# Optimization experiments

Hardware: AMD Instinct MI355X
Metric: run time of the kernel (lower is better)

Reference implementation:

```python
import jax, jax.numpy as jnp
import numpy as np

E = 1024          # embed_dim
BS = 8            # number of sequences (bs = pre_lf_indexs.shape[0])
L = 8192          # tokens per sequence
N = BS * L        # packed tokens
CACHE = 16384     # lf cache rows
EPS = 1e-6


def setup_inputs() -> dict:
    key = jax.random.key(0)
    ks = jax.random.split(key, 9)
    inputs = jax.random.normal(ks[0], (N, E), jnp.float32)
    conv1_weight = jax.random.normal(ks[1], (E, E), jnp.float32) * (1.0 / np.sqrt(E))
    conv2_weight = jax.random.normal(ks[2], (E // 2, 2 * E), jnp.float32) * (1.0 / np.sqrt(E // 2))
    conv1_bias = jax.random.normal(ks[3], (E // 2,), jnp.float32) * 0.02
    conv2_bias = jax.random.normal(ks[4], (E,), jnp.float32) * 0.02
    ln_weight = jnp.ones((E,), jnp.float32)
    lf1_caches = jax.random.normal(ks[5], (CACHE, E), jnp.float32)
    lf2_caches = jax.random.normal(ks[6], (CACHE, E // 2), jnp.float32)
    # packed layout: each sequence prefixed by one cache slot -> T = N + BS rows
    offs = jnp.arange(BS, dtype=jnp.int32) * (L + 1)
    input_lf_loc = offs                                             # cache slot per seq
    inputs_loc = (offs[:, None] + 1 + jnp.arange(L, dtype=jnp.int32)[None, :]).reshape(-1)
    outputs_loc = inputs_loc - 1                                     # 2-tap causal pairing
    out_lf_loc = offs + L                                            # last token of each seq
    pre_lf_indexs = jax.random.randint(ks[7], (BS,), 0, CACHE, jnp.int32)
    out_lf_indexs = jax.random.randint(ks[8], (BS,), 0, CACHE, jnp.int32)
    return {
        'inputs': inputs, 'conv1_weight': conv1_weight, 'conv2_weight': conv2_weight,
        'conv1_bias': conv1_bias, 'conv2_bias': conv2_bias, 'ln_weight': ln_weight,
        'lf1_caches': lf1_caches, 'lf2_caches': lf2_caches,
        'pre_lf_indexs': pre_lf_indexs, 'out_lf_indexs': out_lf_indexs,
        'input_lf_loc': input_lf_loc, 'out_lf_loc': out_lf_loc,
        'inputs_loc': inputs_loc, 'outputs_loc': outputs_loc,
    }


def _fused_cat_conv2d(x, cache, W, pre_idx, in_lf_loc, in_loc, out_loc):
    # scatter cache rows + token rows into the padded buffer [N+bs, D]
    T = x.shape[0] + pre_idx.shape[0]
    xt = jnp.zeros((T, x.shape[1]), x.dtype)
    xt = xt.at[in_lf_loc].set(cache[pre_idx])   # gather from lf cache
    xt = xt.at[in_loc].set(x)
    co = xt @ W                                  # [T, 2*Dout]
    h = co.shape[1] // 2
    # shifted 2-tap causal conv: pair row j (prev) with row j+1 (cur)
    ot = co[:-1, :h] + co[1:, h:]                # [T-1, Dout]
    return ot[out_loc]                           # gather back to token order


def reference(inputs, conv1_weight, conv2_weight, conv1_bias, conv2_bias, ln_weight,
              lf1_caches, lf2_caches, pre_lf_indexs, out_lf_indexs,
              input_lf_loc, out_lf_loc, inputs_loc, outputs_loc):
    # (the index_put_ cache writes in the original are side effects for future
    #  steps only; they do not affect this call's output, so they are omitted)
    output1 = _fused_cat_conv2d(inputs, lf1_caches, conv1_weight,
                                pre_lf_indexs, input_lf_loc, inputs_loc, outputs_loc)
    output1 = output1 + conv1_bias               # [N, E/2]
    output2 = _fused_cat_conv2d(output1, lf2_caches, conv2_weight,
                                pre_lf_indexs, input_lf_loc, inputs_loc, outputs_loc)
    output2 = output2 + conv2_bias               # [N, E]
    x = output2 + inputs                         # residual
    var = jnp.mean(x * x, axis=-1, keepdims=True)
    return x * jax.lax.rsqrt(var + EPS) * ln_weight
```

## Files before the change

### kernel.cpp

```cpp
#include <hip/hip_runtime.h>
#include <hip/hip_bf16.h>


#define EDIM 1024
#define HDIM 512
#define LSEQ 8192
#define BSEQ 8
#define SEQR 8193
#define MTOT (BSEQ * SEQR)
#define XROWS 66048

using v8s = __attribute__((ext_vector_type(8))) short;
using v4f = __attribute__((ext_vector_type(4))) float;

__device__ __forceinline__ unsigned short f2b(float f) {
  union { float f; unsigned u; } v; v.f = f;
  unsigned r = v.u + 0x7fffu + ((v.u >> 16) & 1u);
  return (unsigned short)(r >> 16);
}
__device__ __forceinline__ float b2f(unsigned short h) {
  union { unsigned u; float f; } v; v.u = ((unsigned)h) << 16; return v.f;
}
__device__ __forceinline__ void gl_lds16(const void* g, void* l) {
  __builtin_amdgcn_global_load_lds((const __attribute__((address_space(1))) void*)g,
                                   (__attribute__((address_space(3))) void*)l, 16, 0, 0);
}

__device__ __forceinline__ void trns64(const float* __restrict__ src, int src_ld, int src_c0,
                                       unsigned short* __restrict__ dst, int dst_ld, int dst_k0,
                                       int n0, int k0, float (*t)[65], int tx, int ty) {
#pragma unroll
  for (int yy = 0; yy < 64; yy += 4)
    t[yy + ty][tx] = src[(size_t)(k0 + yy + ty) * src_ld + src_c0 + n0 + tx];
  __syncthreads();
#pragma unroll
  for (int yy = 0; yy < 64; yy += 4)
    dst[(size_t)(n0 + yy + ty) * dst_ld + dst_k0 + k0 + tx] = f2b(t[tx][yy + ty]);
}

__global__ __launch_bounds__(256) void prep_all(const float* __restrict__ W1,
                                                const float* __restrict__ W2,
                                                const float* __restrict__ lf2,
                                                const int* __restrict__ preidx,
                                                unsigned short* __restrict__ W1c,
                                                unsigned short* __restrict__ W2c,
                                                unsigned short* __restrict__ c2b) {
  __shared__ float t[64][65];
  const int bk = blockIdx.x;
  const int tid = threadIdx.x;
  if (bk == 512) {
    for (int c = tid; c < HDIM; c += 256)
#pragma unroll
      for (int b = 0; b < BSEQ; ++b)
        c2b[b * HDIM + c] = f2b(lf2[(size_t)preidx[b] * HDIM + c]);
    return;
  }
  const int tx = tid & 63, ty = tid >> 6;
  const int which = bk >> 7, s = bk & 127;
  if (which == 0)       trns64(W1, 1024, 0,    W1c, 2048, 0,    (s & 7) * 64,  (s >> 3) * 64, t, tx, ty);
  else if (which == 1)  trns64(W1, 1024, 512,  W1c, 2048, 1024, (s & 7) * 64,  (s >> 3) * 64, t, tx, ty);
  else if (which == 2)  trns64(W2, 2048, 0,    W2c, 1024, 0,    (s & 15) * 64, (s >> 4) * 64, t, tx, ty);
  else                  trns64(W2, 2048, 1024, W2c, 1024, 512,  (s & 15) * 64, (s >> 4) * 64, t, tx, ty);
}

__global__ __launch_bounds__(256) void cvt_full(const float* __restrict__ inputs,
                                                const float* __restrict__ lf1,
                                                const int* __restrict__ preidx,
                                                unsigned short* __restrict__ Xbf) {
  const int r = blockIdx.x * 4 + (threadIdx.x >> 6);
  const int lane = threadIdx.x & 63;
  unsigned short* dst = Xbf + (size_t)r * EDIM;
  if (r >= MTOT) {
#pragma unroll
    for (int c = lane * 4; c < EDIM; c += 256)
      *(ushort4*)&dst[c] = (ushort4){0, 0, 0, 0};
    return;
  }
  const int b = r / SEQR, rr = r % SEQR;
  const float* src = (rr == 0) ? (lf1 + (size_t)preidx[b] * EDIM)
                               : (inputs + (size_t)(b * LSEQ + rr - 1) * EDIM);
#pragma unroll
  for (int c = lane * 4; c < EDIM; c += 256) {
    const float4 v = *(const float4*)(src + c);
    *(ushort4*)&dst[c] = (ushort4){f2b(v.x), f2b(v.y), f2b(v.z), f2b(v.w)};
  }
}

__global__ __launch_bounds__(512) void fixup_full(const unsigned short* __restrict__ Xbf,
                                                  const unsigned short* __restrict__ W1c,
                                                  const float* __restrict__ b1,
                                                  const unsigned short* __restrict__ c2b,
                                                  unsigned short* __restrict__ A2) {
  const int blk = blockIdx.x;
  const int tid = threadIdx.x;
  if (blk == 7) {
#pragma unroll
    for (int b = 0; b < BSEQ; ++b)
      A2[(size_t)(b * SEQR) * HDIM + tid] = c2b[b * HDIM + tid];
    return;
  }
  const int r = 65536 + blk;
  const unsigned short* a = Xbf + (size_t)r * EDIM;
  const unsigned short* wrow = W1c + (size_t)tid * 2048;
  float s = 0.f;
  for (int k = 0; k < 2048; k += 8) {
    const v8s av = *(const v8s*)&a[k];
    const v8s wv = *(const v8s*)&wrow[k];
#pragma unroll
    for (int j = 0; j < 8; ++j)
      s += b2f((unsigned short)av[j]) * b2f((unsigned short)wv[j]);
  }
  A2[(size_t)(r + 1) * HDIM + tid] = f2b(s + b1[tid]);
}

#define PHASE(p, boA_, off_, ra_)                                                      \
  {                                                                                    \
    v8s af[2][2];                                                                      \
    _Pragma("unroll") for (int m2 = 0; m2 < 2; ++m2)                                   \
    _Pragma("unroll") for (int kx = 0; kx < 2; ++kx)                                   \
      af[m2][kx] = *(const v8s*)&lds[(boA_) +                                          \
          ((2 * (p) + m2) * 32 + wm * 16 + lr + (off_)) * 64 +                         \
          (((kx * 4 + lk) ^ (ra_)) << 3)];                                             \
    __builtin_amdgcn_s_setprio(1);                                                     \
    _Pragma("unroll") for (int m2 = 0; m2 < 2; ++m2)                                   \
    _Pragma("unroll") for (int nc = 0; nc < 4; ++nc)                                   \
    _Pragma("unroll") for (int kx = 0; kx < 2; ++kx)                                   \
      acc[2 * (p) + m2][nc] = __builtin_amdgcn_mfma_f32_16x16x32_bf16(                 \
          af[m2][kx], bf[nc][kx], acc[2 * (p) + m2][nc], 0, 0, 0);                     \
    __builtin_amdgcn_s_setprio(0);                                                     \
  }

#define LOAD_BFR(boB_)                                                                 \
  _Pragma("unroll") for (int nc = 0; nc < 4; ++nc)                                     \
  _Pragma("unroll") for (int kx = 0; kx < 2; ++kx)                                     \
    bf[nc][kx] = *(const v8s*)&lds[(boB_) + (nc * 64 + wn * 16 + lr) * 64 +            \
                                   (((kx * 4 + lk) ^ ra7a) << 3)];

#define STEP4(boA_, off_, ra_)                                                         \
  PHASE(0, boA_, off_, ra_) PHASE(1, boA_, off_, ra_)                                  \
  PHASE(2, boA_, off_, ra_) PHASE(3, boA_, off_, ra_)

template <int K, int NT, bool SHIFTC, bool AMAP>
__global__ __launch_bounds__(512, 2) void gemm_pair(const unsigned short* __restrict__ A,
                                                    const unsigned short* __restrict__ B,
                                                    unsigned short* __restrict__ C,
                                                    const float* __restrict__ bias,
                                                    int q, int r) {
  constexpr int NH = K / 128;
  constexpr int LDA = K / 2;
  constexpr int N = NT * 256;
  constexpr int A0 = 0, A1 = 16512, B_A = 33024, B_B = 49408;
  __shared__ __align__(16) unsigned short lds[65792];

  const int h = blockIdx.x;
  const int xcd = h & 7, idx = h >> 3;
  const int tsw = (xcd < r ? xcd * (q + 1) : r * (q + 1) + (xcd - r) * q) + idx;
  const int mt = tsw / NT, nt = tsw % NT;
  const size_t m0 = (size_t)mt * 256, n0 = (size_t)nt * 256;
  const int tid = threadIdx.x;
  const int w = tid >> 6, lane = tid & 63;
  const int wm = w >> 2, wn = w & 3;
  const int lr = lane & 15, lk = lane >> 4;
  const int ra7a = lr & 7, ra7b = (lr + 1) & 7;
  const int srow = tid >> 3, slot = tid & 7;
  const int gslot = slot ^ (srow & 7);
  const int dAB = srow * 64 + slot * 8;
  const int aBase = (int)m0 + (AMAP ? ((int)m0 >> 13) : 0);

  auto stageApair = [&](int dstE, int i) {
#pragma unroll
    for (int j = 0; j < 4; ++j) {
      const int rr = j * 64 + (tid >> 3);
      gl_lds16(A + (size_t)(aBase + rr) * LDA + i * 64 + ((tid & 7) ^ (rr & 7)) * 8,
               &lds[dstE + rr * 64 + (tid & 7) * 8]);
    }
    if (tid < 8)
      gl_lds16(A + (size_t)(aBase + 256) * LDA + i * 64 + tid * 8,
               &lds[dstE + 256 * 64 + tid * 8]);
  };
  auto stageB = [&](int dstE, int hh, int t) {
    const unsigned short* s = B + (size_t)(n0 + hh * 128 + srow) * K + t * 64 + gslot * 8;
    unsigned short* d = &lds[dstE + hh * 8192 + dAB];
    gl_lds16(s, d);
    gl_lds16(s + (size_t)64 * K, d + 4096);
  };

  v4f acc[8][4];
#pragma unroll
  for (int i = 0; i < 8; ++i)
#pragma unroll
    for (int j = 0; j < 4; ++j) acc[i][j] = (v4f){0.f, 0.f, 0.f, 0.f};

  stageApair(A0, 0);
  stageB(B_A, 0, 0); stageB(B_A, 1, 0);
  asm volatile("s_waitcnt vmcnt(0)" ::: "memory");
  __builtin_amdgcn_s_barrier();

#pragma unroll 1
  for (int i = 0; i < NH - 1; ++i) {
    const int boA = (i & 1) ? A1 : A0;
    const int soA = (i & 1) ? A0 : A1;
    v8s bf[4][2];
    stageB(B_B, 0, i + NH); stageB(B_B, 1, i + NH);
    stageApair(soA, i + 1);
    LOAD_BFR(B_A)
    STEP4(boA, 0, ra7a)
    asm volatile("s_waitcnt vmcnt(4)" ::: "memory");
    __builtin_amdgcn_s_barrier();
    stageB(B_A, 0, i + 1); stageB(B_A, 1, i + 1);
    LOAD_BFR(B_B)
    STEP4(boA, 1, ra7b)
    asm volatile("s_waitcnt vmcnt(0)" ::: "memory");
    __builtin_amdgcn_s_barrier();
  }
  {
    const int boA = ((NH - 1) & 1) ? A1 : A0;
    v8s bf[4][2];
    stageB(B_B, 0, 2 * NH - 1); stageB(B_B, 1, 2 * NH - 1);
    LOAD_BFR(B_A)
    STEP4(boA, 0, ra7a)
    asm volatile("s_waitcnt vmcnt(0)" ::: "memory");
    __builtin_amdgcn_s_barrier();
    LOAD_BFR(B_B)
    STEP4(boA, 1, ra7b)
  }

#pragma unroll
  for (int mr = 0; mr < 8; ++mr)
#pragma unroll
    for (int nc = 0; nc < 4; ++nc) {
      const size_t col = n0 + nc * 64 + wn * 16 + lr;
      float bv = 0.f;
      if constexpr (SHIFTC) bv = bias[col];
#pragma unroll
      for (int g = 0; g < 4; ++g) {
        const size_t row = m0 + mr * 32 + wm * 16 + lk * 4 + g + (SHIFTC ? 1 : 0);
        C[row * N + col] = f2b(acc[mr][nc][g] + bv);
      }
    }
}

__global__ __launch_bounds__(256) void epilogue_full(
    const unsigned short* __restrict__ Zo, const unsigned short* __restrict__ Xbf,
    const float* __restrict__ b2, const float* __restrict__ lnw,
    float* __restrict__ out) {
  const int u = blockIdx.x;
  const size_t rx = (size_t)u + (u >> 13) + 1;
  const int tid = threadIdx.x;
  const int j0 = tid * 4;

  const ushort4 z = *(const ushort4*)&Zo[(size_t)u * EDIM + j0];
  const ushort4 xb = *(const ushort4*)&Xbf[rx * EDIM + j0];
  const float4 bb = *(const float4*)&b2[j0];
  const float4 lw = *(const float4*)&lnw[j0];

  const float x0 = b2f(z.x) + bb.x + b2f(xb.x);
  const float x1 = b2f(z.y) + bb.y + b2f(xb.y);
  const float x2 = b2f(z.z) + bb.z + b2f(xb.z);
  const float x3 = b2f(z.w) + bb.w + b2f(xb.w);

  float ss = x0 * x0 + x1 * x1 + x2 * x2 + x3 * x3;
#pragma unroll
  for (int o = 32; o > 0; o >>= 1) ss += __shfl_xor(ss, o, 64);
  __shared__ float sp[4];
  if ((tid & 63) == 0) sp[tid >> 6] = ss;
  __syncthreads();
  const float tot = sp[0] + sp[1] + sp[2] + sp[3];
  const float scale = rsqrtf(tot * (1.0f / EDIM) + 1e-6f);

  float4 o4;
  o4.x = x0 * scale * lw.x; o4.y = x1 * scale * lw.y;
  o4.z = x2 * scale * lw.z; o4.w = x3 * scale * lw.w;
  *(float4*)&out[(size_t)u * EDIM + j0] = o4;
}

extern "C" void kernel_launch(void* const* d_in, const int* in_sizes, int n_in,
                              void* d_out, int out_size, void* d_ws, size_t ws_size,
                              hipStream_t stream) {
  const float* inputs = (const float*)d_in[0];
  const float* W1 = (const float*)d_in[1];
  const float* W2 = (const float*)d_in[2];
  const float* b1 = (const float*)d_in[3];
  const float* b2 = (const float*)d_in[4];
  const float* lnw = (const float*)d_in[5];
  const float* lf1 = (const float*)d_in[6];
  const float* lf2 = (const float*)d_in[7];
  const int* preidx = (const int*)d_in[8];
  float* out = (float*)d_out;

  char* ws = (char*)d_ws;
  unsigned short* Xbf = (unsigned short*)(ws);
  unsigned short* A2  = (unsigned short*)(ws + 135266304ULL);
  unsigned short* Zo  = (unsigned short*)(ws + 202899456ULL);
  unsigned short* W1c = (unsigned short*)(ws + 337117184ULL);
  unsigned short* W2c = (unsigned short*)(ws + 339214336ULL);
  unsigned short* c2b = (unsigned short*)(ws + 341311488ULL);

  prep_all<<<513, 256, 0, stream>>>(W1, W2, lf2, preidx, W1c, W2c, c2b);
  cvt_full<<<XROWS / 4, 256, 0, stream>>>(inputs, lf1, preidx, Xbf);
  gemm_pair<2048, 2, true, false><<<512, 512, 0, stream>>>(Xbf, W1c, A2, b1, 64, 0);
  fixup_full<<<8, 512, 0, stream>>>(Xbf, W1c, b1, c2b, A2);
  gemm_pair<1024, 4, false, true><<<1024, 512, 0, stream>>>(A2, W2c, Zo, nullptr, 128, 0);
  epilogue_full<<<BSEQ * LSEQ, 256, 0, stream>>>(Zo, Xbf, b2, lnw, out);
}
```

Before: 471.5 us.

## Interleave global-to-LDS staging with MFMA phases using per-phase barriers

```diff
diff --git a/kernel.cpp b/kernel.cpp
--- a/kernel.cpp
+++ b/kernel.cpp
@@ -113,22 +113,12 @@
   A2[(size_t)(r + 1) * HDIM + tid] = f2b(s + b1[tid]);
 }
 
-#define PHASE(p, boA_, off_, ra_)                                                      \
-  {                                                                                    \
-    v8s af[2][2];                                                                      \
-    _Pragma("unroll") for (int m2 = 0; m2 < 2; ++m2)                                   \
-    _Pragma("unroll") for (int kx = 0; kx < 2; ++kx)                                   \
-      af[m2][kx] = *(const v8s*)&lds[(boA_) +                                          \
-          ((2 * (p) + m2) * 32 + wm * 16 + lr + (off_)) * 64 +                         \
-          (((kx * 4 + lk) ^ (ra_)) << 3)];                                             \
-    __builtin_amdgcn_s_setprio(1);                                                     \
-    _Pragma("unroll") for (int m2 = 0; m2 < 2; ++m2)                                   \
-    _Pragma("unroll") for (int nc = 0; nc < 4; ++nc)                                   \
-    _Pragma("unroll") for (int kx = 0; kx < 2; ++kx)                                   \
-      acc[2 * (p) + m2][nc] = __builtin_amdgcn_mfma_f32_16x16x32_bf16(                 \
-          af[m2][kx], bf[nc][kx], acc[2 * (p) + m2][nc], 0, 0, 0);                     \
-    __builtin_amdgcn_s_setprio(0);                                                     \
-  }
+#define LOAD_AFR(p, boA_, off_, ra_)                                                   \
+  _Pragma("unroll") for (int m2 = 0; m2 < 2; ++m2)                                     \
+  _Pragma("unroll") for (int kx = 0; kx < 2; ++kx)                                     \
+    af[m2][kx] = *(const v8s*)&lds[(boA_) +                                            \
+        ((2 * (p) + m2) * 32 + wm * 16 + lr + (off_)) * 64 +                           \
+        (((kx * 4 + lk) ^ (ra_)) << 3)];
 
 #define LOAD_BFR(boB_)                                                                 \
   _Pragma("unroll") for (int nc = 0; nc < 4; ++nc)                                     \
@@ -136,9 +126,22 @@
     bf[nc][kx] = *(const v8s*)&lds[(boB_) + (nc * 64 + wn * 16 + lr) * 64 +            \
                                    (((kx * 4 + lk) ^ ra7a) << 3)];
 
-#define STEP4(boA_, off_, ra_)                                                         \
-  PHASE(0, boA_, off_, ra_) PHASE(1, boA_, off_, ra_)                                  \
-  PHASE(2, boA_, off_, ra_) PHASE(3, boA_, off_, ra_)
+#define MFMA_CORE(p)                                                                   \
+  __builtin_amdgcn_s_barrier();                                                        \
+  asm volatile("s_waitcnt lgkmcnt(0)" ::: "memory");                                   \
+  __builtin_amdgcn_s_setprio(1);                                                       \
+  _Pragma("unroll") for (int m2 = 0; m2 < 2; ++m2)                                     \
+  _Pragma("unroll") for (int nc = 0; nc < 4; ++nc)                                     \
+  _Pragma("unroll") for (int kx = 0; kx < 2; ++kx)                                     \
+    acc[2 * (p) + m2][nc] = __builtin_amdgcn_mfma_f32_16x16x32_bf16(                   \
+        af[m2][kx], bf[nc][kx], acc[2 * (p) + m2][nc], 0, 0, 0);                       \
+  __builtin_amdgcn_s_setprio(0);
+
+#define MFMA_PH(p)    MFMA_CORE(p) __builtin_amdgcn_s_barrier();
+#define MFMA_PH_W5(p) MFMA_CORE(p)                                                     \
+  asm volatile("s_waitcnt vmcnt(5)" ::: "memory"); __builtin_amdgcn_s_barrier();
+#define MFMA_PH_W0(p) MFMA_CORE(p)                                                     \
+  asm volatile("s_waitcnt vmcnt(0)" ::: "memory"); __builtin_amdgcn_s_barrier();
 
 template <int K, int NT, bool SHIFTC, bool AMAP>
 __global__ __launch_bounds__(512, 2) void gemm_pair(const unsigned short* __restrict__ A,
@@ -167,16 +170,24 @@
   const int dAB = srow * 64 + slot * 8;
   const int aBase = (int)m0 + (AMAP ? ((int)m0 >> 13) : 0);
 
-  auto stageApair = [&](int dstE, int i) {
-#pragma unroll
-    for (int j = 0; j < 4; ++j) {
+  auto stageA01 = [&](int dstE, int i) {
+#pragma unroll
+    for (int j = 0; j < 2; ++j) {
       const int rr = j * 64 + (tid >> 3);
       gl_lds16(A + (size_t)(aBase + rr) * LDA + i * 64 + ((tid & 7) ^ (rr & 7)) * 8,
                &lds[dstE + rr * 64 + (tid & 7) * 8]);
     }
-    if (tid < 8)
-      gl_lds16(A + (size_t)(aBase + 256) * LDA + i * 64 + tid * 8,
-               &lds[dstE + 256 * 64 + tid * 8]);
+  };
+  auto stageA23t = [&](int dstE, int i) {
+#pragma unroll
+    for (int j = 2; j < 4; ++j) {
+      const int rr = j * 64 + (tid >> 3);
+      gl_lds16(A + (size_t)(aBase + rr) * LDA + i * 64 + ((tid & 7) ^ (rr & 7)) * 8,
+               &lds[dstE + rr * 64 + (tid & 7) * 8]);
+    }
+    if ((tid & 63) < 8)
+      gl_lds16(A + (size_t)(aBase + 256) * LDA + i * 64 + (tid & 7) * 8,
+               &lds[dstE + 256 * 64 + (tid & 7) * 8]);
   };
   auto stageB = [&](int dstE, int hh, int t) {
     const unsigned short* s = B + (size_t)(n0 + hh * 128 + srow) * K + t * 64 + gslot * 8;
@@ -191,7 +202,7 @@
 #pragma unroll
     for (int j = 0; j < 4; ++j) acc[i][j] = (v4f){0.f, 0.f, 0.f, 0.f};
 
-  stageApair(A0, 0);
+  stageA01(A0, 0); stageA23t(A0, 0);
   stageB(B_A, 0, 0); stageB(B_A, 1, 0);
   asm volatile("s_waitcnt vmcnt(0)" ::: "memory");
   __builtin_amdgcn_s_barrier();
@@ -200,29 +211,55 @@
   for (int i = 0; i < NH - 1; ++i) {
     const int boA = (i & 1) ? A1 : A0;
     const int soA = (i & 1) ? A0 : A1;
-    v8s bf[4][2];
-    stageB(B_B, 0, i + NH); stageB(B_B, 1, i + NH);
-    stageApair(soA, i + 1);
+    v8s bf[4][2], af[2][2];
     LOAD_BFR(B_A)
-    STEP4(boA, 0, ra7a)
-    asm volatile("s_waitcnt vmcnt(4)" ::: "memory");
-    __builtin_amdgcn_s_barrier();
-    stageB(B_A, 0, i + 1); stageB(B_A, 1, i + 1);
+    LOAD_AFR(0, boA, 0, ra7a)
+    stageB(B_B, 0, i + NH);
+    MFMA_PH(0)
+    LOAD_AFR(1, boA, 0, ra7a)
+    stageB(B_B, 1, i + NH);
+    MFMA_PH(1)
+    LOAD_AFR(2, boA, 0, ra7a)
+    stageA01(soA, i + 1);
+    MFMA_PH(2)
+    LOAD_AFR(3, boA, 0, ra7a)
+    stageA23t(soA, i + 1);
+    MFMA_PH_W5(3)
     LOAD_BFR(B_B)
-    STEP4(boA, 1, ra7b)
-    asm volatile("s_waitcnt vmcnt(0)" ::: "memory");
-    __builtin_amdgcn_s_barrier();
+    LOAD_AFR(0, boA, 1, ra7b)
+    stageB(B_A, 0, i + 1);
+    MFMA_PH(0)
+    LOAD_AFR(1, boA, 1, ra7b)
+    stageB(B_A, 1, i + 1);
+    MFMA_PH(1)
+    LOAD_AFR(2, boA, 1, ra7b)
+    MFMA_PH(2)
+    LOAD_AFR(3, boA, 1, ra7b)
+    MFMA_PH_W0(3)
   }
   {
     const int boA = ((NH - 1) & 1) ? A1 : A0;
-    v8s bf[4][2];
-    stageB(B_B, 0, 2 * NH - 1); stageB(B_B, 1, 2 * NH - 1);
+    v8s bf[4][2], af[2][2];
     LOAD_BFR(B_A)
-    STEP4(boA, 0, ra7a)
-    asm volatile("s_waitcnt vmcnt(0)" ::: "memory");
-    __builtin_amdgcn_s_barrier();
+    LOAD_AFR(0, boA, 0, ra7a)
+    stageB(B_B, 0, 2 * NH - 1);
+    MFMA_PH(0)
+    LOAD_AFR(1, boA, 0, ra7a)
+    stageB(B_B, 1, 2 * NH - 1);
+    MFMA_PH(1)
+    LOAD_AFR(2, boA, 0, ra7a)
+    MFMA_PH(2)
+    LOAD_AFR(3, boA, 0, ra7a)
+    MFMA_PH_W0(3)
     LOAD_BFR(B_B)
-    STEP4(boA, 1, ra7b)
+    LOAD_AFR(0, boA, 1, ra7b)
+    MFMA_PH(0)
+    LOAD_AFR(1, boA, 1, ra7b)
+    MFMA_PH(1)
+    LOAD_AFR(2, boA, 1, ra7b)
+    MFMA_PH(2)
+    LOAD_AFR(3, boA, 1, ra7b)
+    MFMA_PH(3)
   }
 
 #pragma unroll
```

Measured after the change: 475.3 us. Within noise of the previous version (+0.8%).

## Fuse fp32-to-bf16 input conversion and cache gather into first GEMM A-loading

Applied to the files above, without the earlier changes.

```diff
diff --git a/kernel.cpp b/kernel.cpp
--- a/kernel.cpp
+++ b/kernel.cpp
@@ -63,30 +63,7 @@
   else                  trns64(W2, 2048, 1024, W2c, 1024, 512,  (s & 15) * 64, (s >> 4) * 64, t, tx, ty);
 }
 
-__global__ __launch_bounds__(256) void cvt_full(const float* __restrict__ inputs,
-                                                const float* __restrict__ lf1,
-                                                const int* __restrict__ preidx,
-                                                unsigned short* __restrict__ Xbf) {
-  const int r = blockIdx.x * 4 + (threadIdx.x >> 6);
-  const int lane = threadIdx.x & 63;
-  unsigned short* dst = Xbf + (size_t)r * EDIM;
-  if (r >= MTOT) {
-#pragma unroll
-    for (int c = lane * 4; c < EDIM; c += 256)
-      *(ushort4*)&dst[c] = (ushort4){0, 0, 0, 0};
-    return;
-  }
-  const int b = r / SEQR, rr = r % SEQR;
-  const float* src = (rr == 0) ? (lf1 + (size_t)preidx[b] * EDIM)
-                               : (inputs + (size_t)(b * LSEQ + rr - 1) * EDIM);
-#pragma unroll
-  for (int c = lane * 4; c < EDIM; c += 256) {
-    const float4 v = *(const float4*)(src + c);
-    *(ushort4*)&dst[c] = (ushort4){f2b(v.x), f2b(v.y), f2b(v.z), f2b(v.w)};
-  }
-}
-
-__global__ __launch_bounds__(512) void fixup_full(const unsigned short* __restrict__ Xbf,
+__global__ __launch_bounds__(512) void fixup_full(const float* __restrict__ inputs,
                                                   const unsigned short* __restrict__ W1c,
                                                   const float* __restrict__ b1,
                                                   const unsigned short* __restrict__ c2b,
@@ -100,17 +77,174 @@
     return;
   }
   const int r = 65536 + blk;
-  const unsigned short* a = Xbf + (size_t)r * EDIM;
+  const float* x0 = inputs + (size_t)(r - 8) * EDIM;
+  const float* x1 = inputs + (size_t)(r - 7) * EDIM;
   const unsigned short* wrow = W1c + (size_t)tid * 2048;
   float s = 0.f;
-  for (int k = 0; k < 2048; k += 8) {
-    const v8s av = *(const v8s*)&a[k];
-    const v8s wv = *(const v8s*)&wrow[k];
-#pragma unroll
-    for (int j = 0; j < 8; ++j)
-      s += b2f((unsigned short)av[j]) * b2f((unsigned short)wv[j]);
+  for (int k = 0; k < 1024; k += 4) {
+    const float4 a = *(const float4*)(x0 + k);
+    const float4 c = *(const float4*)(x1 + k);
+    const ushort4 wa = *(const ushort4*)&wrow[k];
+    const ushort4 wc = *(const ushort4*)&wrow[1024 + k];
+    s += b2f(f2b(a.x)) * b2f(wa.x) + b2f(f2b(a.y)) * b2f(wa.y) +
+         b2f(f2b(a.z)) * b2f(wa.z) + b2f(f2b(a.w)) * b2f(wa.w);
+    s += b2f(f2b(c.x)) * b2f(wc.x) + b2f(f2b(c.y)) * b2f(wc.y) +
+         b2f(f2b(c.z)) * b2f(wc.z) + b2f(f2b(c.w)) * b2f(wc.w);
   }
   A2[(size_t)(r + 1) * HDIM + tid] = f2b(s + b1[tid]);
+}
+
+#define KX1(kx, boA_, off_, ra_, boB_)                                          \
+  {                                                                             \
+    v8s bfk[4], afk[2];                                                         \
+    _Pragma("unroll") for (int nc = 0; nc < 4; ++nc)                            \
+      bfk[nc] = *(const v8s*)&lds[(boB_) + (nc * 64 + wn * 16 + lr) * 64 +      \
+                                  ((((kx)*4 + lk) ^ ra7a) << 3)];               \
+    _Pragma("unroll") for (int p = 0; p < 4; ++p) {                             \
+      _Pragma("unroll") for (int m2 = 0; m2 < 2; ++m2)                          \
+        afk[m2] = *(const v8s*)&lds[(boA_) +                                    \
+            ((2 * p + m2) * 32 + wm * 16 + lr + (off_)) * 64 +                  \
+            ((((kx)*4 + lk) ^ (ra_)) << 3)];                                    \
+      __builtin_amdgcn_s_setprio(1);                                            \
+      _Pragma("unroll") for (int m2 = 0; m2 < 2; ++m2)                          \
+      _Pragma("unroll") for (int nc = 0; nc < 4; ++nc)                          \
+        acc[2 * p + m2][nc] = __builtin_amdgcn_mfma_f32_16x16x32_bf16(          \
+            afk[m2], bfk[nc], acc[2 * p + m2][nc], 0, 0, 0);                    \
+      __builtin_amdgcn_s_setprio(0);                                            \
+    }                                                                           \
+  }
+
+__global__ __launch_bounds__(512, 2) void gemm1_f32(const float* __restrict__ X,
+                                                    const float* __restrict__ lf1,
+                                                    const int* __restrict__ preidx,
+                                                    const unsigned short* __restrict__ B,
+                                                    unsigned short* __restrict__ C,
+                                                    const float* __restrict__ bias,
+                                                    int q, int r) {
+  constexpr int K = 2048, NH = 16, NT = 2, N = 512;
+  constexpr int A0 = 0, A1 = 16512, B_A = 33024, B_B = 49408;
+  __shared__ __align__(16) unsigned short lds[65792];
+
+  const int h = blockIdx.x;
+  const int xcd = h & 7, idx = h >> 3;
+  const int tsw = (xcd < r ? xcd * (q + 1) : r * (q + 1) + (xcd - r) * q) + idx;
+  const int mt = tsw / NT, nt = tsw % NT;
+  const size_t m0 = (size_t)mt * 256, n0 = (size_t)nt * 256;
+  const int tid = threadIdx.x;
+  const int w = tid >> 6, lane = tid & 63;
+  const int wm = w >> 2, wn = w & 3;
+  const int lr = lane & 15, lk = lane >> 4;
+  const int ra7a = lr & 7, ra7b = (lr + 1) & 7;
+  const int srow = tid >> 3, slot = tid & 7;
+  const int gslot = slot ^ (srow & 7);
+  const int dAB = srow * 64 + slot * 8;
+  const unsigned short* bSrc = B + (size_t)(n0 + srow) * K + gslot * 8;
+
+  const int myrow = tid >> 3;
+  const int fcol = slot * 8;
+  const float* abase[4];
+#pragma unroll
+  for (int j = 0; j < 4; ++j) {
+    const int u = (int)m0 + j * 64 + myrow;
+    int b = u >> 13; int rr = u - b * SEQR;
+    if (rr < 0) { b--; rr += SEQR; }
+    abase[j] = (rr == 0) ? (lf1 + (size_t)preidx[b] * EDIM)
+                         : (X + (size_t)(u - b - 1) * EDIM);
+  }
+  const float* tbase = nullptr;
+  if (tid < 8) {
+    const int u = (int)m0 + 256;
+    int b = u >> 13; int rr = u - b * SEQR;
+    if (rr < 0) { b--; rr += SEQR; }
+    tbase = (rr == 0) ? (lf1 + (size_t)preidx[b] * EDIM)
+                      : (X + (size_t)(u - b - 1) * EDIM);
+  }
+
+  auto ldrow = [&](const float* bp, int i, float4& a, float4& bq) {
+    const float* p = bp + i * 64 + fcol;
+    a = *(const float4*)p; bq = *(const float4*)(p + 4);
+  };
+  auto wrrow = [&](int dstE, int rloc, const float4& a, const float4& bq) {
+    v8s pk;
+    pk[0] = (short)f2b(a.x);  pk[1] = (short)f2b(a.y);
+    pk[2] = (short)f2b(a.z);  pk[3] = (short)f2b(a.w);
+    pk[4] = (short)f2b(bq.x); pk[5] = (short)f2b(bq.y);
+    pk[6] = (short)f2b(bq.z); pk[7] = (short)f2b(bq.w);
+    *(v8s*)&lds[dstE + rloc * 64 + ((slot ^ (rloc & 7)) << 3)] = pk;
+  };
+  auto stageB = [&](int dstE, int hh, int t) {
+    const unsigned short* s = bSrc + (size_t)(hh * 128) * K + (size_t)t * 64;
+    unsigned short* d = &lds[dstE + hh * 8192 + dAB];
+    gl_lds16(s, d);
+    gl_lds16(s + (size_t)64 * K, d + 4096);
+  };
+
+  v4f acc[8][4];
+#pragma unroll
+  for (int i = 0; i < 8; ++i)
+#pragma unroll
+    for (int j = 0; j < 4; ++j) acc[i][j] = (v4f){0.f, 0.f, 0.f, 0.f};
+
+  {
+    float4 a0, b0;
+#pragma unroll
+    for (int j = 0; j < 4; ++j) { ldrow(abase[j], 0, a0, b0); wrrow(A0, j * 64 + myrow, a0, b0); }
+    if (tid < 8) { ldrow(tbase, 0, a0, b0); wrrow(A0, 256, a0, b0); }
+    stageB(B_A, 0, 0); stageB(B_A, 1, 0);
+  }
+  __syncthreads();
+
+#pragma unroll 1
+  for (int i = 0; i < NH - 1; ++i) {
+    const int boA = (i & 1) ? A1 : A0;
+    const int soA = (i & 1) ? A0 : A1;
+    stageB(B_B, 0, i + NH); stageB(B_B, 1, i + NH);
+    float4 la0, lb0, la1, lb1;
+    ldrow(abase[0], i + 1, la0, lb0);
+    ldrow(abase[1], i + 1, la1, lb1);
+    KX1(0, boA, 0, ra7a, B_A)
+    wrrow(soA, 0 * 64 + myrow, la0, lb0);
+    wrrow(soA, 1 * 64 + myrow, la1, lb1);
+    ldrow(abase[2], i + 1, la0, lb0);
+    ldrow(abase[3], i + 1, la1, lb1);
+    float4 ta = {0, 0, 0, 0}, tb = {0, 0, 0, 0};
+    if (tid < 8) ldrow(tbase, i + 1, ta, tb);
+    KX1(1, boA, 0, ra7a, B_A)
+    wrrow(soA, 2 * 64 + myrow, la0, lb0);
+    wrrow(soA, 3 * 64 + myrow, la1, lb1);
+    if (tid < 8) wrrow(soA, 256, ta, tb);
+    asm volatile("s_waitcnt vmcnt(0)" ::: "memory");
+    __builtin_amdgcn_s_barrier();
+    stageB(B_A, 0, i + 1); stageB(B_A, 1, i + 1);
+    KX1(0, boA, 1, ra7b, B_B)
+    KX1(1, boA, 1, ra7b, B_B)
+    asm volatile("s_waitcnt vmcnt(0)" ::: "memory");
+    asm volatile("s_waitcnt lgkmcnt(0)" ::: "memory");
+    __builtin_amdgcn_s_barrier();
+  }
+  {
+    const int boA = ((NH - 1) & 1) ? A1 : A0;
+    stageB(B_B, 0, 2 * NH - 1); stageB(B_B, 1, 2 * NH - 1);
+    KX1(0, boA, 0, ra7a, B_A)
+    KX1(1, boA, 0, ra7a, B_A)
+    asm volatile("s_waitcnt vmcnt(0)" ::: "memory");
+    __builtin_amdgcn_s_barrier();
+    KX1(0, boA, 1, ra7b, B_B)
+    KX1(1, boA, 1, ra7b, B_B)
+  }
+
+#pragma unroll
+  for (int mr = 0; mr < 8; ++mr)
+#pragma unroll
+    for (int nc = 0; nc < 4; ++nc) {
+      const size_t col = n0 + nc * 64 + wn * 16 + lr;
+      const float bv = bias[col];
+#pragma unroll
+      for (int g = 0; g < 4; ++g) {
+        const size_t row = m0 + mr * 32 + wm * 16 + lk * 4 + g + 1;
+        C[row * N + col] = f2b(acc[mr][nc][g] + bv);
+      }
+    }
 }
 
 #define PHASE(p, boA_, off_, ra_)                                                      \
@@ -241,23 +375,22 @@
 }
 
 __global__ __launch_bounds__(256) void epilogue_full(
-    const unsigned short* __restrict__ Zo, const unsigned short* __restrict__ Xbf,
+    const unsigned short* __restrict__ Zo, const float* __restrict__ inputs,
     const float* __restrict__ b2, const float* __restrict__ lnw,
     float* __restrict__ out) {
   const int u = blockIdx.x;
-  const size_t rx = (size_t)u + (u >> 13) + 1;
   const int tid = threadIdx.x;
   const int j0 = tid * 4;
 
   const ushort4 z = *(const ushort4*)&Zo[(size_t)u * EDIM + j0];
-  const ushort4 xb = *(const ushort4*)&Xbf[rx * EDIM + j0];
+  const float4 inp = *(const float4*)&inputs[(size_t)u * EDIM + j0];
   const float4 bb = *(const float4*)&b2[j0];
   const float4 lw = *(const float4*)&lnw[j0];
 
-  const float x0 = b2f(z.x) + bb.x + b2f(xb.x);
-  const float x1 = b2f(z.y) + bb.y + b2f(xb.y);
-  const float x2 = b2f(z.z) + bb.z + b2f(xb.z);
-  const float x3 = b2f(z.w) + bb.w + b2f(xb.w);
+  const float x0 = b2f(z.x) + bb.x + inp.x;
+  const float x1 = b2f(z.y) + bb.y + inp.y;
+  const float x2 = b2f(z.z) + bb.z + inp.z;
+  const float x3 = b2f(z.w) + bb.w + inp.w;
 
   float ss = x0 * x0 + x1 * x1 + x2 * x2 + x3 * x3;
 #pragma unroll
@@ -289,17 +422,15 @@
   float* out = (float*)d_out;
 
   char* ws = (char*)d_ws;
-  unsigned short* Xbf = (unsigned short*)(ws);
-  unsigned short* A2  = (unsigned short*)(ws + 135266304ULL);
-  unsigned short* Zo  = (unsigned short*)(ws + 202899456ULL);
-  unsigned short* W1c = (unsigned short*)(ws + 337117184ULL);
-  unsigned short* W2c = (unsigned short*)(ws + 339214336ULL);
-  unsigned short* c2b = (unsigned short*)(ws + 341311488ULL);
+  unsigned short* A2  = (unsigned short*)(ws);
+  unsigned short* Zo  = (unsigned short*)(ws + 67633152ULL);
+  unsigned short* W1c = (unsigned short*)(ws + 201850880ULL);
+  unsigned short* W2c = (unsigned short*)(ws + 203948032ULL);
+  unsigned short* c2b = (unsigned short*)(ws + 206045184ULL);
 
   prep_all<<<513, 256, 0, stream>>>(W1, W2, lf2, preidx, W1c, W2c, c2b);
-  cvt_full<<<XROWS / 4, 256, 0, stream>>>(inputs, lf1, preidx, Xbf);
-  gemm_pair<2048, 2, true, false><<<512, 512, 0, stream>>>(Xbf, W1c, A2, b1, 64, 0);
-  fixup_full<<<8, 512, 0, stream>>>(Xbf, W1c, b1, c2b, A2);
+  gemm1_f32<<<512, 512, 0, stream>>>(inputs, lf1, preidx, W1c, A2, b1, 64, 0);
+  fixup_full<<<8, 512, 0, stream>>>(inputs, W1c, b1, c2b, A2);
   gemm_pair<1024, 4, false, true><<<1024, 512, 0, stream>>>(A2, W2c, Zo, nullptr, 128, 0);
-  epilogue_full<<<BSEQ * LSEQ, 256, 0, stream>>>(Zo, Xbf, b2, lnw, out);
-}
+  epilogue_full<<<BSEQ * LSEQ, 256, 0, stream>>>(Zo, inputs, b2, lnw, out);
+}
```

New measurement: 706.0 us. 1.5x slower.

## Shrink GEMM tiles to 128x128 with 256-thread blocks

Applied to the files above, without the earlier changes.

```diff
diff --git a/kernel.cpp b/kernel.cpp
--- a/kernel.cpp
+++ b/kernel.cpp
@@ -115,25 +115,23 @@
 
 #define PHASE(p, boA_, off_, ra_)                                                      \
   {                                                                                    \
-    v8s af[2][2];                                                                      \
-    _Pragma("unroll") for (int m2 = 0; m2 < 2; ++m2)                                   \
+    v8s af[2];                                                                         \
     _Pragma("unroll") for (int kx = 0; kx < 2; ++kx)                                   \
-      af[m2][kx] = *(const v8s*)&lds[(boA_) +                                          \
-          ((2 * (p) + m2) * 32 + wm * 16 + lr + (off_)) * 64 +                         \
+      af[kx] = *(const v8s*)&lds[(boA_) +                                              \
+          ((p) * 32 + wm * 16 + lr + (off_)) * 64 +                                    \
           (((kx * 4 + lk) ^ (ra_)) << 3)];                                             \
     __builtin_amdgcn_s_setprio(1);                                                     \
-    _Pragma("unroll") for (int m2 = 0; m2 < 2; ++m2)                                   \
     _Pragma("unroll") for (int nc = 0; nc < 4; ++nc)                                   \
     _Pragma("unroll") for (int kx = 0; kx < 2; ++kx)                                   \
-      acc[2 * (p) + m2][nc] = __builtin_amdgcn_mfma_f32_16x16x32_bf16(                 \
-          af[m2][kx], bf[nc][kx], acc[2 * (p) + m2][nc], 0, 0, 0);                     \
+      acc[p][nc] = __builtin_amdgcn_mfma_f32_16x16x32_bf16(                            \
+          af[kx], bf[nc][kx], acc[p][nc], 0, 0, 0);                                    \
     __builtin_amdgcn_s_setprio(0);                                                     \
   }
 
 #define LOAD_BFR(boB_)                                                                 \
   _Pragma("unroll") for (int nc = 0; nc < 4; ++nc)                                     \
   _Pragma("unroll") for (int kx = 0; kx < 2; ++kx)                                     \
-    bf[nc][kx] = *(const v8s*)&lds[(boB_) + (nc * 64 + wn * 16 + lr) * 64 +            \
+    bf[nc][kx] = *(const v8s*)&lds[(boB_) + (wn * 64 + nc * 16 + lr) * 64 +            \
                                    (((kx * 4 + lk) ^ ra7a) << 3)];
 
 #define STEP4(boA_, off_, ra_)                                                         \
@@ -141,58 +139,59 @@
   PHASE(2, boA_, off_, ra_) PHASE(3, boA_, off_, ra_)
 
 template <int K, int NT, bool SHIFTC, bool AMAP>
-__global__ __launch_bounds__(512, 2) void gemm_pair(const unsigned short* __restrict__ A,
-                                                    const unsigned short* __restrict__ B,
-                                                    unsigned short* __restrict__ C,
-                                                    const float* __restrict__ bias,
-                                                    int q, int r) {
+__global__ __launch_bounds__(256, 2) void gemm_pair128(const unsigned short* __restrict__ A,
+                                                       const unsigned short* __restrict__ B,
+                                                       unsigned short* __restrict__ C,
+                                                       const float* __restrict__ bias,
+                                                       int q, int r) {
   constexpr int NH = K / 128;
   constexpr int LDA = K / 2;
-  constexpr int N = NT * 256;
-  constexpr int A0 = 0, A1 = 16512, B_A = 33024, B_B = 49408;
-  __shared__ __align__(16) unsigned short lds[65792];
+  constexpr int N = NT * 128;
+  constexpr int A0 = 0, A1 = 8256, B_A = 16512, B_B = 24704;
+  __shared__ __align__(16) unsigned short lds[32896];
 
   const int h = blockIdx.x;
   const int xcd = h & 7, idx = h >> 3;
   const int tsw = (xcd < r ? xcd * (q + 1) : r * (q + 1) + (xcd - r) * q) + idx;
   const int mt = tsw / NT, nt = tsw % NT;
-  const size_t m0 = (size_t)mt * 256, n0 = (size_t)nt * 256;
+  const size_t m0 = (size_t)mt * 128, n0 = (size_t)nt * 128;
   const int tid = threadIdx.x;
   const int w = tid >> 6, lane = tid & 63;
-  const int wm = w >> 2, wn = w & 3;
+  const int wm = w >> 1, wn = w & 1;
   const int lr = lane & 15, lk = lane >> 4;
   const int ra7a = lr & 7, ra7b = (lr + 1) & 7;
   const int srow = tid >> 3, slot = tid & 7;
   const int gslot = slot ^ (srow & 7);
-  const int dAB = srow * 64 + slot * 8;
   const int aBase = (int)m0 + (AMAP ? ((int)m0 >> 13) : 0);
 
   auto stageApair = [&](int dstE, int i) {
 #pragma unroll
     for (int j = 0; j < 4; ++j) {
-      const int rr = j * 64 + (tid >> 3);
-      gl_lds16(A + (size_t)(aBase + rr) * LDA + i * 64 + ((tid & 7) ^ (rr & 7)) * 8,
-               &lds[dstE + rr * 64 + (tid & 7) * 8]);
+      const int rr = j * 32 + srow;
+      gl_lds16(A + (size_t)(aBase + rr) * LDA + i * 64 + gslot * 8,
+               &lds[dstE + rr * 64 + slot * 8]);
     }
     if (tid < 8)
-      gl_lds16(A + (size_t)(aBase + 256) * LDA + i * 64 + tid * 8,
-               &lds[dstE + 256 * 64 + tid * 8]);
+      gl_lds16(A + (size_t)(aBase + 128) * LDA + i * 64 + tid * 8,
+               &lds[dstE + 128 * 64 + tid * 8]);
   };
-  auto stageB = [&](int dstE, int hh, int t) {
-    const unsigned short* s = B + (size_t)(n0 + hh * 128 + srow) * K + t * 64 + gslot * 8;
-    unsigned short* d = &lds[dstE + hh * 8192 + dAB];
-    gl_lds16(s, d);
-    gl_lds16(s + (size_t)64 * K, d + 4096);
+  auto stageB = [&](int dstE, int t) {
+#pragma unroll
+    for (int j = 0; j < 4; ++j) {
+      const int row = j * 32 + srow;
+      gl_lds16(B + (size_t)(n0 + row) * K + (size_t)t * 64 + gslot * 8,
+               &lds[dstE + row * 64 + slot * 8]);
+    }
   };
 
-  v4f acc[8][4];
-#pragma unroll
-  for (int i = 0; i < 8; ++i)
+  v4f acc[4][4];
+#pragma unroll
+  for (int i = 0; i < 4; ++i)
 #pragma unroll
     for (int j = 0; j < 4; ++j) acc[i][j] = (v4f){0.f, 0.f, 0.f, 0.f};
 
   stageApair(A0, 0);
-  stageB(B_A, 0, 0); stageB(B_A, 1, 0);
+  stageB(B_A, 0);
   asm volatile("s_waitcnt vmcnt(0)" ::: "memory");
   __builtin_amdgcn_s_barrier();
 
@@ -201,13 +200,13 @@
     const int boA = (i & 1) ? A1 : A0;
     const int soA = (i & 1) ? A0 : A1;
     v8s bf[4][2];
-    stageB(B_B, 0, i + NH); stageB(B_B, 1, i + NH);
+    stageB(B_B, i + NH);
     stageApair(soA, i + 1);
     LOAD_BFR(B_A)
     STEP4(boA, 0, ra7a)
     asm volatile("s_waitcnt vmcnt(4)" ::: "memory");
     __builtin_amdgcn_s_barrier();
-    stageB(B_A, 0, i + 1); stageB(B_A, 1, i + 1);
+    stageB(B_A, i + 1);
     LOAD_BFR(B_B)
     STEP4(boA, 1, ra7b)
     asm volatile("s_waitcnt vmcnt(0)" ::: "memory");
@@ -216,7 +215,7 @@
   {
     const int boA = ((NH - 1) & 1) ? A1 : A0;
     v8s bf[4][2];
-    stageB(B_B, 0, 2 * NH - 1); stageB(B_B, 1, 2 * NH - 1);
+    stageB(B_B, 2 * NH - 1);
     LOAD_BFR(B_A)
     STEP4(boA, 0, ra7a)
     asm volatile("s_waitcnt vmcnt(0)" ::: "memory");
@@ -226,10 +225,10 @@
   }
 
 #pragma unroll
-  for (int mr = 0; mr < 8; ++mr)
+  for (int mr = 0; mr < 4; ++mr)
 #pragma unroll
     for (int nc = 0; nc < 4; ++nc) {
-      const size_t col = n0 + nc * 64 + wn * 16 + lr;
+      const size_t col = n0 + wn * 64 + nc * 16 + lr;
       float bv = 0.f;
       if constexpr (SHIFTC) bv = bias[col];
 #pragma unroll
@@ -298,8 +297,8 @@
 
   prep_all<<<513, 256, 0, stream>>>(W1, W2, lf2, preidx, W1c, W2c, c2b);
   cvt_full<<<XROWS / 4, 256, 0, stream>>>(inputs, lf1, preidx, Xbf);
-  gemm_pair<2048, 2, true, false><<<512, 512, 0, stream>>>(Xbf, W1c, A2, b1, 64, 0);
+  gemm_pair128<2048, 4, true, false><<<2048, 256, 0, stream>>>(Xbf, W1c, A2, b1, 256, 0);
   fixup_full<<<8, 512, 0, stream>>>(Xbf, W1c, b1, c2b, A2);
-  gemm_pair<1024, 4, false, true><<<1024, 512, 0, stream>>>(A2, W2c, Zo, nullptr, 128, 0);
+  gemm_pair128<1024, 8, false, true><<<4096, 256, 0, stream>>>(A2, W2c, Zo, nullptr, 512, 0);
   epilogue_full<<<BSEQ * LSEQ, 256, 0, stream>>>(Zo, Xbf, b2, lnw, out);
 }
```

After: 489.2 us. 1.04x slower.
